# Kernel optimization log

Measured on AMD Instinct MI355X. Metric: run time of the kernel, lower is better.

The kernel has to match this reference:

```python
import jax, jax.numpy as jnp
import numpy as np

D_MODEL = 1024
D_FF = 4096


def _layernorm(x, gamma, beta, eps=1e-5):
    mu = jnp.mean(x, axis=-1, keepdims=True)
    var = jnp.var(x, axis=-1, keepdims=True)
    return (x - mu) * jax.lax.rsqrt(var + eps) * gamma + beta


def setup_inputs() -> dict:
    key = jax.random.key(0)
    ks = jax.random.split(key, 7)
    B, S = 4, 2048
    src = jax.random.normal(ks[0], (B, S, D_MODEL), dtype=jnp.float32)
    gamma1 = jnp.ones((D_MODEL,), jnp.float32)
    beta1 = jnp.zeros((D_MODEL,), jnp.float32)
    gamma2 = jnp.ones((D_MODEL,), jnp.float32)
    beta2 = jnp.zeros((D_MODEL,), jnp.float32)
    w1 = jax.random.normal(ks[1], (D_MODEL, D_FF), jnp.float32) * (1.0 / np.sqrt(D_MODEL))
    b1 = jnp.zeros((D_FF,), jnp.float32)
    w2 = jax.random.normal(ks[2], (D_FF, D_MODEL), jnp.float32) * (1.0 / np.sqrt(D_FF))
    b2 = jnp.zeros((D_MODEL,), jnp.float32)
    return {"src": src, "gamma1": gamma1, "beta1": beta1,
            "gamma2": gamma2, "beta2": beta2,
            "w1": w1, "b1": b1, "w2": w2, "b2": b2}


def reference(src, gamma1, beta1, gamma2, beta2, w1, b1, w2, b2):
    # Pre-LN self-attention (single head, Q=K=V=norm_x, no projections)
    norm_x = _layernorm(src, gamma1, beta1)
    dim_k = norm_x.shape[-1]
    scores = jnp.einsum('bqd,bkd->bqk', norm_x, norm_x) / jnp.sqrt(jnp.float32(dim_k))
    weights = jax.nn.softmax(scores, axis=-1)
    attn = jnp.einsum('bqk,bkd->bqd', weights, norm_x)
    x = src + attn  # dropout p=0 -> identity
    # Pre-LN FFN
    h = _layernorm(x, gamma2, beta2)
    h = jax.nn.gelu(h @ w1 + b1, approximate=False)
    h = h @ w2 + b2
    return h + x
```

## Files before the change

kernel.cpp:

```cpp
#include <hip/hip_runtime.h>
#include <hip/hip_bf16.h>
#include <math.h>

typedef __attribute__((ext_vector_type(8))) short s8vec;
typedef __attribute__((ext_vector_type(4))) float f32x4;
typedef __attribute__((ext_vector_type(4))) unsigned short us4;

__device__ __forceinline__ unsigned short f2bf(float f) {
  unsigned u = __float_as_uint(f);
  u = (u + 0x7fffu + ((u >> 16) & 1u)) >> 16;
  return (unsigned short)u;
}
__device__ __forceinline__ float bf2f(unsigned short u) {
  return __uint_as_float(((unsigned)u) << 16);
}

__device__ __forceinline__ float fast_gelu(float t) {
  float t2 = t * t;
  float u = t * (1.59576912f + 0.07135481f * t2);
  float e = __expf(-u);
  return t * __frcp_rn(1.0f + e);
}

__device__ __forceinline__ void async_ld16(const unsigned short* g, unsigned short* l) {
  __builtin_amdgcn_global_load_lds(
      (__attribute__((address_space(1))) void*)g,
      (__attribute__((address_space(3))) void*)l, 16, 0, 0);
}

template <int EPI>
__global__ __launch_bounds__(256) void gemm_nt(
    const unsigned short* __restrict__ A, const unsigned short* __restrict__ B,
    float* __restrict__ outF, unsigned short* __restrict__ outB,
    const float* __restrict__ bias, const float* __restrict__ res,
    int M, int N, int K,
    long long bA, long long bB, long long bO, long long bR, float scale)
{
  __shared__ __align__(16) unsigned short As[128 * 64];
  __shared__ __align__(16) unsigned short Bs[128 * 64];

  const int tid = threadIdx.x;
  const int w = tid >> 6;
  const int l = tid & 63;
  const int z = blockIdx.z;

  A += (size_t)z * bA;
  B += (size_t)z * bB;

  const size_t tileM = (size_t)blockIdx.y * 128;
  const size_t tileN = (size_t)blockIdx.x * 128;

  const int sRow = l >> 3;
  const int sChunk = (l & 7) ^ sRow;
  const unsigned short* aBase = A + (tileM + (w << 5) + sRow) * (size_t)K + (sChunk << 3);
  const unsigned short* bBase = B + (tileN + (w << 5) + sRow) * (size_t)K + (sChunk << 3);
  unsigned short* ldsA = &As[(w << 5) * 64];
  unsigned short* ldsB = &Bs[(w << 5) * 64];

  const int wm = (w >> 1) << 6;
  const int wn = (w & 1) << 6;
  const int fr = l & 15;
  const int fq = l >> 4;

  f32x4 acc[4][4] = {};

  for (int k0 = 0; k0 < K; k0 += 64) {
    __syncthreads();
#pragma unroll
    for (int i = 0; i < 4; ++i) {
      async_ld16(aBase + k0 + (size_t)(i << 3) * K, ldsA + (i << 3) * 64);
      async_ld16(bBase + k0 + (size_t)(i << 3) * K, ldsB + (i << 3) * 64);
    }
    __syncthreads();

#pragma unroll
    for (int kk = 0; kk < 2; ++kk) {
      s8vec af[4], bf[4];
#pragma unroll
      for (int i = 0; i < 4; ++i) {
        const int R = wm + (i << 4) + fr;
        const int p = ((kk << 2) + fq) ^ (fr & 7);
        af[i] = *(const s8vec*)&As[R * 64 + (p << 3)];
      }
#pragma unroll
      for (int j = 0; j < 4; ++j) {
        const int R = wn + (j << 4) + fr;
        const int p = ((kk << 2) + fq) ^ (fr & 7);
        bf[j] = *(const s8vec*)&Bs[R * 64 + (p << 3)];
      }
#pragma unroll
      for (int i = 0; i < 4; ++i)
#pragma unroll
        for (int j = 0; j < 4; ++j)
          acc[i][j] = __builtin_amdgcn_mfma_f32_16x16x32_bf16(af[i], bf[j], acc[i][j], 0, 0, 0);
    }
  }

  float* oF = outF + (size_t)z * bO;
  unsigned short* oB = outB + (size_t)z * bO;
  const float* rs = res + (size_t)z * bR;

  float bcol[4];
  if (EPI >= 2) {
#pragma unroll
    for (int j = 0; j < 4; ++j) bcol[j] = bias[tileN + wn + (j << 4) + fr];
  }

#pragma unroll
  for (int i = 0; i < 4; ++i) {
#pragma unroll
    for (int r = 0; r < 4; ++r) {
      const size_t row = tileM + wm + (i << 4) + (fq << 2) + r;
      const size_t rb = row * (size_t)N;
#pragma unroll
      for (int j = 0; j < 4; ++j) {
        const size_t col = tileN + wn + (j << 4) + fr;
        const float v = acc[i][j][r];
        if (EPI == 0) {
          oF[rb + col] = v * scale;
        } else if (EPI == 1) {
          oF[rb + col] = v + rs[rb + col];
        } else if (EPI == 2) {
          oB[rb + col] = f2bf(fast_gelu(v + bcol[j]));
        } else {
          oF[rb + col] = v + bcol[j] + rs[rb + col];
        }
      }
    }
  }
}

__global__ __launch_bounds__(256) void ln_row(
    const float* __restrict__ x, const float* __restrict__ gamma,
    const float* __restrict__ beta, unsigned short* __restrict__ out)
{
  const int row = blockIdx.x;
  const float4* xr = (const float4*)(x + (size_t)row * 1024);
  const int tid = threadIdx.x;
  float4 v = xr[tid];
  float s = v.x + v.y + v.z + v.w;
  float q = v.x * v.x + v.y * v.y + v.z * v.z + v.w * v.w;
#pragma unroll
  for (int off = 32; off > 0; off >>= 1) {
    s += __shfl_down(s, off);
    q += __shfl_down(q, off);
  }
  __shared__ float rs_[4], rq_[4];
  const int w = tid >> 6, l = tid & 63;
  if (l == 0) { rs_[w] = s; rq_[w] = q; }
  __syncthreads();
  s = rs_[0] + rs_[1] + rs_[2] + rs_[3];
  q = rq_[0] + rq_[1] + rq_[2] + rq_[3];
  const float mu = s * (1.0f / 1024.0f);
  const float var = q * (1.0f / 1024.0f) - mu * mu;
  const float rstd = rsqrtf(var + 1e-5f);
  const float4 g = ((const float4*)gamma)[tid];
  const float4 b = ((const float4*)beta)[tid];
  us4 o;
  o.x = f2bf((v.x - mu) * rstd * g.x + b.x);
  o.y = f2bf((v.y - mu) * rstd * g.y + b.y);
  o.z = f2bf((v.z - mu) * rstd * g.z + b.z);
  o.w = f2bf((v.w - mu) * rstd * g.w + b.w);
  ((us4*)(out + (size_t)row * 1024))[tid] = o;
}

__global__ __launch_bounds__(256) void softmax_row(
    const float* __restrict__ sc, unsigned short* __restrict__ pr)
{
  const int row = blockIdx.x;
  const float4* s4 = (const float4*)(sc + (size_t)row * 2048);
  const int tid = threadIdx.x;
  float4 a = s4[tid], b = s4[tid + 256];
  float mx = fmaxf(fmaxf(fmaxf(a.x, a.y), fmaxf(a.z, a.w)),
                   fmaxf(fmaxf(b.x, b.y), fmaxf(b.z, b.w)));
#pragma unroll
  for (int off = 32; off > 0; off >>= 1) mx = fmaxf(mx, __shfl_down(mx, off));
  __shared__ float red[4];
  const int w = tid >> 6, l = tid & 63;
  if (l == 0) red[w] = mx;
  __syncthreads();
  mx = fmaxf(fmaxf(red[0], red[1]), fmaxf(red[2], red[3]));
  __syncthreads();
  float e[8];
  e[0] = __expf(a.x - mx); e[1] = __expf(a.y - mx);
  e[2] = __expf(a.z - mx); e[3] = __expf(a.w - mx);
  e[4] = __expf(b.x - mx); e[5] = __expf(b.y - mx);
  e[6] = __expf(b.z - mx); e[7] = __expf(b.w - mx);
  float s = e[0] + e[1] + e[2] + e[3] + e[4] + e[5] + e[6] + e[7];
#pragma unroll
  for (int off = 32; off > 0; off >>= 1) s += __shfl_down(s, off);
  if (l == 0) red[w] = s;
  __syncthreads();
  s = red[0] + red[1] + red[2] + red[3];
  const float inv = 1.0f / s;
  us4 o0, o1;
  o0.x = f2bf(e[0] * inv); o0.y = f2bf(e[1] * inv);
  o0.z = f2bf(e[2] * inv); o0.w = f2bf(e[3] * inv);
  o1.x = f2bf(e[4] * inv); o1.y = f2bf(e[5] * inv);
  o1.z = f2bf(e[6] * inv); o1.w = f2bf(e[7] * inv);
  us4* out4 = (us4*)(pr + (size_t)row * 2048);
  out4[tid] = o0;
  out4[tid + 256] = o1;
}

template <bool BF16IN>
__global__ __launch_bounds__(256) void transpose_conv(
    const void* __restrict__ in_, unsigned short* __restrict__ out,
    int R, int C, long long bIn, long long bOut)
{
  __shared__ float tile[32][33];
  const int z = blockIdx.z;
  const int tx = threadIdx.x, ty = threadIdx.y;
  const int c0 = blockIdx.x * 32, r0 = blockIdx.y * 32;
  if (BF16IN) {
    const unsigned short* in = (const unsigned short*)in_ + (size_t)z * bIn;
    for (int i = ty; i < 32; i += 8)
      tile[i][tx] = bf2f(in[(size_t)(r0 + i) * C + c0 + tx]);
  } else {
    const float* in = (const float*)in_ + (size_t)z * bIn;
    for (int i = ty; i < 32; i += 8)
      tile[i][tx] = in[(size_t)(r0 + i) * C + c0 + tx];
  }
  __syncthreads();
  unsigned short* o = out + (size_t)z * bOut;
  for (int i = ty; i < 32; i += 8)
    o[(size_t)(c0 + i) * R + r0 + tx] = f2bf(tile[tx][i]);
}

extern "C" void kernel_launch(void* const* d_in, const int* in_sizes, int n_in,
                              void* d_out, int out_size, void* d_ws, size_t ws_size,
                              hipStream_t stream)
{
  (void)in_sizes; (void)n_in; (void)out_size; (void)ws_size;
  const float* src = (const float*)d_in[0];
  const float* g1  = (const float*)d_in[1];
  const float* be1 = (const float*)d_in[2];
  const float* g2  = (const float*)d_in[3];
  const float* be2 = (const float*)d_in[4];
  const float* w1  = (const float*)d_in[5];
  const float* b1  = (const float*)d_in[6];
  const float* w2  = (const float*)d_in[7];
  const float* b2  = (const float*)d_in[8];
  float* out = (float*)d_out;

  char* ws = (char*)d_ws;
  const size_t SZ_NORMX  = (size_t)8192 * 1024 * 2;
  const size_t SZ_SCORES = (size_t)4 * 2048 * 2048 * 4;
  const size_t SZ_PROBS  = (size_t)4 * 2048 * 2048 * 2;
  const size_t SZ_X      = (size_t)8192 * 1024 * 4;
  const size_t SZ_W1T    = (size_t)1024 * 4096 * 2;

  unsigned short* normx  = (unsigned short*)(ws);
  unsigned short* normxT = (unsigned short*)(ws + SZ_NORMX);
  float*          scores = (float*)(ws + 2 * SZ_NORMX);
  unsigned short* probs  = (unsigned short*)(ws + 2 * SZ_NORMX + SZ_SCORES);
  float*          xbuf   = (float*)(ws + 2 * SZ_NORMX + SZ_SCORES + SZ_PROBS);
  unsigned short* w1t    = (unsigned short*)(ws + 2 * SZ_NORMX + SZ_SCORES + SZ_PROBS + SZ_X);
  unsigned short* w2t    = (unsigned short*)(ws + 2 * SZ_NORMX + SZ_SCORES + SZ_PROBS + SZ_X + SZ_W1T);
  unsigned short* normx2 = normx;
  unsigned short* hbuf   = (unsigned short*)scores;

  const dim3 tb(32, 8);
  transpose_conv<false><<<dim3(128, 32, 1), tb, 0, stream>>>(w1, w1t, 1024, 4096, 0, 0);
  transpose_conv<false><<<dim3(32, 128, 1), tb, 0, stream>>>(w2, w2t, 4096, 1024, 0, 0);

  ln_row<<<8192, 256, 0, stream>>>(src, g1, be1, normx);
  transpose_conv<true><<<dim3(32, 64, 4), tb, 0, stream>>>(
      normx, normxT, 2048, 1024, (long long)2048 * 1024, (long long)1024 * 2048);

  gemm_nt<0><<<dim3(16, 16, 4), 256, 0, stream>>>(
      normx, normx, scores, nullptr, nullptr, nullptr,
      2048, 2048, 1024,
      (long long)2048 * 1024, (long long)2048 * 1024, (long long)2048 * 2048, 0, 0.03125f);

  softmax_row<<<8192, 256, 0, stream>>>(scores, probs);

  gemm_nt<1><<<dim3(8, 16, 4), 256, 0, stream>>>(
      probs, normxT, xbuf, nullptr, nullptr, src,
      2048, 1024, 2048,
      (long long)2048 * 2048, (long long)1024 * 2048, (long long)2048 * 1024,
      (long long)2048 * 1024, 1.0f);

  ln_row<<<8192, 256, 0, stream>>>(xbuf, g2, be2, normx2);

  gemm_nt<2><<<dim3(32, 64, 1), 256, 0, stream>>>(
      normx2, w1t, nullptr, hbuf, b1, nullptr,
      8192, 4096, 1024, 0, 0, 0, 0, 1.0f);

  gemm_nt<3><<<dim3(8, 64, 1), 256, 0, stream>>>(
      hbuf, w2t, out, nullptr, b2, xbuf,
      8192, 1024, 4096, 0, 0, 0, 0, 1.0f);
}
```

Baseline: 466.6 us.

## Switch GEMM to 32x32x16 MFMA and store attention scores as bf16

```diff
diff --git a/kernel.cpp b/kernel.cpp
--- a/kernel.cpp
+++ b/kernel.cpp
@@ -3,7 +3,7 @@
 #include <math.h>
 
 typedef __attribute__((ext_vector_type(8))) short s8vec;
-typedef __attribute__((ext_vector_type(4))) float f32x4;
+typedef __attribute__((ext_vector_type(16))) float f32x16;
 typedef __attribute__((ext_vector_type(4))) unsigned short us4;
 
 __device__ __forceinline__ unsigned short f2bf(float f) {
@@ -59,10 +59,10 @@
 
   const int wm = (w >> 1) << 6;
   const int wn = (w & 1) << 6;
-  const int fr = l & 15;
-  const int fq = l >> 4;
-
-  f32x4 acc[4][4] = {};
+  const int fr = l & 31;
+  const int fq = l >> 5;
+
+  f32x16 acc[2][2] = {};
 
   for (int k0 = 0; k0 < K; k0 += 64) {
     __syncthreads();
@@ -74,25 +74,20 @@
     __syncthreads();
 
 #pragma unroll
-    for (int kk = 0; kk < 2; ++kk) {
-      s8vec af[4], bf[4];
-#pragma unroll
-      for (int i = 0; i < 4; ++i) {
-        const int R = wm + (i << 4) + fr;
-        const int p = ((kk << 2) + fq) ^ (fr & 7);
-        af[i] = *(const s8vec*)&As[R * 64 + (p << 3)];
-      }
-#pragma unroll
-      for (int j = 0; j < 4; ++j) {
-        const int R = wn + (j << 4) + fr;
-        const int p = ((kk << 2) + fq) ^ (fr & 7);
-        bf[j] = *(const s8vec*)&Bs[R * 64 + (p << 3)];
-      }
-#pragma unroll
-      for (int i = 0; i < 4; ++i)
-#pragma unroll
-        for (int j = 0; j < 4; ++j)
-          acc[i][j] = __builtin_amdgcn_mfma_f32_16x16x32_bf16(af[i], bf[j], acc[i][j], 0, 0, 0);
+    for (int s = 0; s < 4; ++s) {
+      const int p = ((s << 1) + fq) ^ (fr & 7);
+      s8vec af[2], bf[2];
+#pragma unroll
+      for (int i = 0; i < 2; ++i)
+        af[i] = *(const s8vec*)&As[(wm + (i << 5) + fr) * 64 + (p << 3)];
+#pragma unroll
+      for (int j = 0; j < 2; ++j)
+        bf[j] = *(const s8vec*)&Bs[(wn + (j << 5) + fr) * 64 + (p << 3)];
+#pragma unroll
+      for (int i = 0; i < 2; ++i)
+#pragma unroll
+        for (int j = 0; j < 2; ++j)
+          acc[i][j] = __builtin_amdgcn_mfma_f32_32x32x16_bf16(af[i], bf[j], acc[i][j], 0, 0, 0);
     }
   }
 
@@ -100,24 +95,24 @@
   unsigned short* oB = outB + (size_t)z * bO;
   const float* rs = res + (size_t)z * bR;
 
-  float bcol[4];
+  float bcol[2];
   if (EPI >= 2) {
 #pragma unroll
-    for (int j = 0; j < 4; ++j) bcol[j] = bias[tileN + wn + (j << 4) + fr];
-  }
-
-#pragma unroll
-  for (int i = 0; i < 4; ++i) {
-#pragma unroll
-    for (int r = 0; r < 4; ++r) {
-      const size_t row = tileM + wm + (i << 4) + (fq << 2) + r;
+    for (int j = 0; j < 2; ++j) bcol[j] = bias[tileN + wn + (j << 5) + fr];
+  }
+
+#pragma unroll
+  for (int i = 0; i < 2; ++i) {
+#pragma unroll
+    for (int r = 0; r < 16; ++r) {
+      const size_t row = tileM + wm + (i << 5) + (r & 3) + ((r >> 2) << 3) + (fq << 2);
       const size_t rb = row * (size_t)N;
 #pragma unroll
-      for (int j = 0; j < 4; ++j) {
-        const size_t col = tileN + wn + (j << 4) + fr;
+      for (int j = 0; j < 2; ++j) {
+        const size_t col = tileN + wn + (j << 5) + fr;
         const float v = acc[i][j][r];
         if (EPI == 0) {
-          oF[rb + col] = v * scale;
+          oB[rb + col] = f2bf(v * scale);
         } else if (EPI == 1) {
           oF[rb + col] = v + rs[rb + col];
         } else if (EPI == 2) {
@@ -165,14 +160,18 @@
 }
 
 __global__ __launch_bounds__(256) void softmax_row(
-    const float* __restrict__ sc, unsigned short* __restrict__ pr)
+    const unsigned short* __restrict__ sc, unsigned short* __restrict__ pr)
 {
   const int row = blockIdx.x;
-  const float4* s4 = (const float4*)(sc + (size_t)row * 2048);
+  const s8vec* s8 = (const s8vec*)(sc + (size_t)row * 2048);
   const int tid = threadIdx.x;
-  float4 a = s4[tid], b = s4[tid + 256];
-  float mx = fmaxf(fmaxf(fmaxf(a.x, a.y), fmaxf(a.z, a.w)),
-                   fmaxf(fmaxf(b.x, b.y), fmaxf(b.z, b.w)));
+  s8vec a = s8[tid];
+  float x[8];
+#pragma unroll
+  for (int i = 0; i < 8; ++i) x[i] = bf2f((unsigned short)a[i]);
+  float mx = x[0];
+#pragma unroll
+  for (int i = 1; i < 8; ++i) mx = fmaxf(mx, x[i]);
 #pragma unroll
   for (int off = 32; off > 0; off >>= 1) mx = fmaxf(mx, __shfl_down(mx, off));
   __shared__ float red[4];
@@ -181,26 +180,19 @@
   __syncthreads();
   mx = fmaxf(fmaxf(red[0], red[1]), fmaxf(red[2], red[3]));
   __syncthreads();
-  float e[8];
-  e[0] = __expf(a.x - mx); e[1] = __expf(a.y - mx);
-  e[2] = __expf(a.z - mx); e[3] = __expf(a.w - mx);
-  e[4] = __expf(b.x - mx); e[5] = __expf(b.y - mx);
-  e[6] = __expf(b.z - mx); e[7] = __expf(b.w - mx);
-  float s = e[0] + e[1] + e[2] + e[3] + e[4] + e[5] + e[6] + e[7];
+  float e[8], s = 0.f;
+#pragma unroll
+  for (int i = 0; i < 8; ++i) { e[i] = __expf(x[i] - mx); s += e[i]; }
 #pragma unroll
   for (int off = 32; off > 0; off >>= 1) s += __shfl_down(s, off);
   if (l == 0) red[w] = s;
   __syncthreads();
   s = red[0] + red[1] + red[2] + red[3];
   const float inv = 1.0f / s;
-  us4 o0, o1;
-  o0.x = f2bf(e[0] * inv); o0.y = f2bf(e[1] * inv);
-  o0.z = f2bf(e[2] * inv); o0.w = f2bf(e[3] * inv);
-  o1.x = f2bf(e[4] * inv); o1.y = f2bf(e[5] * inv);
-  o1.z = f2bf(e[6] * inv); o1.w = f2bf(e[7] * inv);
-  us4* out4 = (us4*)(pr + (size_t)row * 2048);
-  out4[tid] = o0;
-  out4[tid + 256] = o1;
+  s8vec o;
+#pragma unroll
+  for (int i = 0; i < 8; ++i) o[i] = (short)f2bf(e[i] * inv);
+  ((s8vec*)(pr + (size_t)row * 2048))[tid] = o;
 }
 
 template <bool BF16IN>
@@ -252,13 +244,13 @@
 
   unsigned short* normx  = (unsigned short*)(ws);
   unsigned short* normxT = (unsigned short*)(ws + SZ_NORMX);
-  float*          scores = (float*)(ws + 2 * SZ_NORMX);
+  unsigned short* scores = (unsigned short*)(ws + 2 * SZ_NORMX);
   unsigned short* probs  = (unsigned short*)(ws + 2 * SZ_NORMX + SZ_SCORES);
   float*          xbuf   = (float*)(ws + 2 * SZ_NORMX + SZ_SCORES + SZ_PROBS);
   unsigned short* w1t    = (unsigned short*)(ws + 2 * SZ_NORMX + SZ_SCORES + SZ_PROBS + SZ_X);
   unsigned short* w2t    = (unsigned short*)(ws + 2 * SZ_NORMX + SZ_SCORES + SZ_PROBS + SZ_X + SZ_W1T);
   unsigned short* normx2 = normx;
-  unsigned short* hbuf   = (unsigned short*)scores;
+  unsigned short* hbuf   = scores;
 
   const dim3 tb(32, 8);
   transpose_conv<false><<<dim3(128, 32, 1), tb, 0, stream>>>(w1, w1t, 1024, 4096, 0, 0);
@@ -269,7 +261,7 @@
       normx, normxT, 2048, 1024, (long long)2048 * 1024, (long long)1024 * 2048);
 
   gemm_nt<0><<<dim3(16, 16, 4), 256, 0, stream>>>(
-      normx, normx, scores, nullptr, nullptr, nullptr,
+      normx, normx, nullptr, scores, nullptr, nullptr,
       2048, 2048, 1024,
       (long long)2048 * 1024, (long long)2048 * 1024, (long long)2048 * 2048, 0, 0.03125f);
 
```

Result: faster. 440.2 us (-5.6%).
